# Performance work log

Measured on AMD Instinct MI355X. Metric: run time of the kernel, lower is better.

## Reference

```python
import jax, jax.numpy as jnp
import numpy as np

IN_C, OUT_C, MX, MY = 64, 64, 32, 32
B, H, W = 16, 256, 256


def setup_inputs() -> dict:
    key = jax.random.key(0)
    k1, k2, k3 = jax.random.split(key, 3)
    scale = 1.0 / (IN_C * OUT_C)
    x = jax.random.normal(k1, (B, IN_C, H, W), dtype=jnp.float32)
    weight_real = scale * jax.random.normal(k2, (IN_C, OUT_C, MX, MY), dtype=jnp.float32)
    weight_imag = scale * jax.random.normal(k3, (IN_C, OUT_C, MX, MY), dtype=jnp.float32)
    return {"x": x, "weight_real": weight_real, "weight_imag": weight_imag}


def reference(x, weight_real, weight_imag):
    Bv, C, Hv, Wv = x.shape
    x_ft = jnp.fft.rfft2(x, norm="ortho")  # [B, C_in, H, W//2+1] complex64
    mx = min(MX, Hv)
    my = min(MY, Wv // 2 + 1)
    x_crop = x_ft[:, :, :mx, :my]
    w = (weight_real[:, :, :mx, :my] + 1j * weight_imag[:, :, :mx, :my]).astype(jnp.complex64)
    # complex contraction over in_channels: [B,i,x,y] x [i,o,x,y] -> [B,o,x,y]
    out_modes = jnp.einsum("bixy,ioxy->boxy", x_crop, w)
    out_ft = jnp.zeros((Bv, OUT_C, Hv, Wv // 2 + 1), dtype=jnp.complex64)
    out_ft = out_ft.at[:, :, :mx, :my].set(out_modes)
    return jnp.fft.irfft2(out_ft, s=(Hv, Wv), norm="ortho")
```

## Files before the change

### kernel.cpp

```cpp
#include <hip/hip_runtime.h>
#include <math.h>


typedef _Float16 f16x4 __attribute__((ext_vector_type(4)));
typedef _Float16 f16x8 __attribute__((ext_vector_type(8)));
typedef float f32x4 __attribute__((ext_vector_type(4)));

__global__ __launch_bounds__(256) void k_tables(float* __restrict__ ws) {
    int idx = blockIdx.x * 256 + threadIdx.x;
    const float STEP = 6.283185307179586f / 256.f;
    float s, c;
    {
        int kx = idx >> 8, h = idx & 255;
        int t = (kx * h) & 255;
        sincosf((float)t * STEP, &s, &c);
        ((float2*)(ws + 16384))[kx * 256 + h] = make_float2(c, s);
    }
    _Float16* e1h = (_Float16*)ws;
    _Float16* e1l = (_Float16*)(ws + 8192);
    _Float16* e2h = (_Float16*)(ws + 32768);
    _Float16* e2l = (_Float16*)(ws + 40960);
    if (idx < 2048) {
        int l = idx & 63, nt = (idx >> 6) & 3, kt = idx >> 8;
        int col = nt * 16 + (l & 15);
        int ky = col >> 1;
        int kb = kt * 32 + (l >> 4) * 8;
#pragma unroll
        for (int j = 0; j < 8; ++j) {
            int k = kb + j;
            int tt_ = (k * ky) & 255;
            sincosf((float)tt_ * STEP, &s, &c);
            float val = ((col & 1) ? -s : c) * 256.f;
            _Float16 h = (_Float16)val;
            e1h[idx * 8 + j] = h;
            e1l[idx * 8 + j] = (_Float16)(val - (float)h);
        }
    } else if (idx < 4096) {
        int i2 = idx - 2048;
        int l = i2 & 63, nt = (i2 >> 6) & 15, kt = i2 >> 10;
        int w = nt * 16 + (l & 15);
        int kb = kt * 32 + (l >> 4) * 8;
#pragma unroll
        for (int j = 0; j < 8; ++j) {
            int k = kb + j;
            int ky = k >> 1;
            int tt_ = (ky * w) & 255;
            sincosf((float)tt_ * STEP, &s, &c);
            float val = ((k & 1) ? -s : c) * 256.f;
            _Float16 h = (_Float16)val;
            e2h[i2 * 8 + j] = h;
            e2l[i2 * 8 + j] = (_Float16)(val - (float)h);
        }
    }
}

__global__ __launch_bounds__(256) void k_f1(const float* __restrict__ x,
                                            const _Float16* __restrict__ e1h,
                                            const _Float16* __restrict__ e1l,
                                            float* __restrict__ y) {
    __shared__ _Float16 Ah[128 * 40];
    __shared__ _Float16 Al[128 * 40];
    int t = threadIdx.x, lane = t & 63, wv = t >> 6;
    long row0 = (long)blockIdx.x * 128;
    f32x4 acc[2][4];
#pragma unroll
    for (int m = 0; m < 2; ++m)
#pragma unroll
        for (int n = 0; n < 4; ++n) acc[m][n] = (f32x4){0.f, 0.f, 0.f, 0.f};
    int abase = (wv * 32 + (lane & 15)) * 40 + (lane >> 4) * 8;

    for (int kt = 0; kt < 8; ++kt) {
#pragma unroll
        for (int n = 0; n < 4; ++n) {
            int f4 = t + n * 256;
            int r = f4 >> 3, c4 = f4 & 7;
            float4 v = *(const float4*)&x[(row0 + r) * 256 + kt * 32 + c4 * 4];
            float s0 = v.x * 256.f, s1 = v.y * 256.f, s2 = v.z * 256.f, s3 = v.w * 256.f;
            _Float16 h0 = (_Float16)s0, h1 = (_Float16)s1;
            _Float16 h2 = (_Float16)s2, h3 = (_Float16)s3;
            *(f16x4*)&Ah[r * 40 + c4 * 4] = (f16x4){h0, h1, h2, h3};
            *(f16x4*)&Al[r * 40 + c4 * 4] =
                (f16x4){(_Float16)(s0 - (float)h0), (_Float16)(s1 - (float)h1),
                        (_Float16)(s2 - (float)h2), (_Float16)(s3 - (float)h3)};
        }
        __syncthreads();
        f16x8 ah0 = *(const f16x8*)&Ah[abase];
        f16x8 ah1 = *(const f16x8*)&Ah[abase + 16 * 40];
        f16x8 al0 = *(const f16x8*)&Al[abase];
        f16x8 al1 = *(const f16x8*)&Al[abase + 16 * 40];
#pragma unroll
        for (int n = 0; n < 4; ++n) {
            f16x8 bh = *(const f16x8*)(e1h + ((kt * 4 + n) * 64 + lane) * 8);
            f16x8 bl = *(const f16x8*)(e1l + ((kt * 4 + n) * 64 + lane) * 8);
            acc[0][n] = __builtin_amdgcn_mfma_f32_16x16x32_f16(ah0, bh, acc[0][n], 0, 0, 0);
            acc[0][n] = __builtin_amdgcn_mfma_f32_16x16x32_f16(al0, bh, acc[0][n], 0, 0, 0);
            acc[0][n] = __builtin_amdgcn_mfma_f32_16x16x32_f16(ah0, bl, acc[0][n], 0, 0, 0);
            acc[1][n] = __builtin_amdgcn_mfma_f32_16x16x32_f16(ah1, bh, acc[1][n], 0, 0, 0);
            acc[1][n] = __builtin_amdgcn_mfma_f32_16x16x32_f16(al1, bh, acc[1][n], 0, 0, 0);
            acc[1][n] = __builtin_amdgcn_mfma_f32_16x16x32_f16(ah1, bl, acc[1][n], 0, 0, 0);
        }
        __syncthreads();
    }
    const float SC = 1.f / 16777216.f;
#pragma unroll
    for (int m = 0; m < 2; ++m)
#pragma unroll
        for (int n = 0; n < 4; ++n)
#pragma unroll
            for (int r = 0; r < 4; ++r) {
                long row = row0 + wv * 32 + m * 16 + (lane >> 4) * 4 + r;
                y[row * 64 + n * 16 + (lane & 15)] = acc[m][n][r] * SC;
            }
}

__global__ __launch_bounds__(256) void k_f2(const float2* __restrict__ tt,
                                            const float2* __restrict__ y,
                                            float2* __restrict__ xf) {
    __shared__ float smem[2176 + 2048];
    float* As = smem;
    float* Bs = smem + 2176;
    int t = threadIdx.x, tx = t & 15, ty = t >> 4;
    int batch = blockIdx.x;
    const float2* ybase = y + (long)batch * 256 * 32;
    float acc[4][4];
#pragma unroll
    for (int i = 0; i < 4; ++i)
#pragma unroll
        for (int j = 0; j < 4; ++j) acc[i][j] = 0.f;

    for (int ht = 0; ht < 8; ++ht) {
        int h0 = ht * 32;
#pragma unroll
        for (int n = 0; n < 4; ++n) {
            int i2 = t + n * 256;
            int kx = i2 >> 5, hh = i2 & 31;
            float2 cs = tt[kx * 256 + h0 + hh];
            As[hh * 68 + kx] = cs.x;
            As[hh * 68 + 32 + kx] = cs.y;
        }
#pragma unroll
        for (int n = 0; n < 4; ++n) {
            int i2 = t + n * 256;
            int hh = i2 >> 5, ky = i2 & 31;
            float2 v = ybase[(h0 + hh) * 32 + ky];
            *(float2*)&Bs[hh * 64 + 2 * ky] = v;
        }
        __syncthreads();
#pragma unroll
        for (int kk = 0; kk < 32; ++kk) {
            float4 a0 = *(const float4*)&As[kk * 68 + ty * 4];
            float4 b0 = *(const float4*)&Bs[kk * 64 + tx * 4];
            float av[4] = {a0.x, a0.y, a0.z, a0.w};
            float bv[4] = {b0.x, b0.y, b0.z, b0.w};
#pragma unroll
            for (int i = 0; i < 4; ++i)
#pragma unroll
                for (int j = 0; j < 4; ++j)
                    acc[i][j] = fmaf(av[i], bv[j], acc[i][j]);
        }
        __syncthreads();
    }
    float* Cs = smem;
#pragma unroll
    for (int i = 0; i < 4; ++i)
#pragma unroll
        for (int j = 0; j < 4; ++j)
            Cs[(ty * 4 + i) * 65 + tx * 4 + j] = acc[i][j];
    __syncthreads();
#pragma unroll
    for (int n = 0; n < 4; ++n) {
        int idx = t + n * 256;
        int kx = idx >> 5, ky = idx & 31;
        float re = Cs[kx * 65 + 2 * ky]     + Cs[(kx + 32) * 65 + 2 * ky + 1];
        float im = Cs[kx * 65 + 2 * ky + 1] - Cs[(kx + 32) * 65 + 2 * ky];
        xf[(long)batch * 1024 + kx * 32 + ky] = make_float2(re, im);
    }
}

__global__ __launch_bounds__(256) void k_mix(const float* __restrict__ wr,
                                             const float* __restrict__ wi,
                                             const float2* __restrict__ xf,
                                             float2* __restrict__ om) {
    __shared__ float2 xs[64 * 32];
    int t = threadIdx.x;
    int b = blockIdx.x >> 5, kx = blockIdx.x & 31;
#pragma unroll
    for (int n = 0; n < 8; ++n) {
        int i2 = t + n * 256;
        int i = i2 >> 5, ky = i2 & 31;
        xs[i2] = xf[(long)(b * 64 + i) * 1024 + kx * 32 + ky];
    }
    __syncthreads();
    int ky = t & 31, og = t >> 5;
    float ar[8], ai[8];
#pragma unroll
    for (int j = 0; j < 8; ++j) { ar[j] = 0.f; ai[j] = 0.f; }
    const float* wrb = wr + kx * 32 + ky;
    const float* wib = wi + kx * 32 + ky;
    for (int i = 0; i < 64; ++i) {
        float2 xv = xs[i * 32 + ky];
#pragma unroll
        for (int j = 0; j < 8; ++j) {
            int o = og * 8 + j;
            long woff = (long)(i * 64 + o) * 1024;
            float wrv = wrb[woff], wiv = wib[woff];
            ar[j] = fmaf(xv.x, wrv, fmaf(-xv.y, wiv, ar[j]));
            ai[j] = fmaf(xv.x, wiv, fmaf(xv.y, wrv, ai[j]));
        }
    }
    float2* omb = om + (long)(b * 64) * 1024 + kx * 32 + ky;
#pragma unroll
    for (int j = 0; j < 8; ++j) {
        int o = og * 8 + j;
        omb[(long)o * 1024] = make_float2(ar[j], ai[j]);
    }
}

__global__ __launch_bounds__(256) void k_i1(const float2* __restrict__ tt,
                                            const float2* __restrict__ om,
                                            float2* __restrict__ g) {
    __shared__ float As[64 * 68];
    __shared__ float Bs[64 * 64];
    int t = threadIdx.x, tx = t & 15, ty = t >> 4;
    int bo = blockIdx.x >> 2, hb = blockIdx.x & 3;
    int h0 = hb * 64;
#pragma unroll
    for (int n = 0; n < 8; ++n) {
        int i2 = t + n * 256;
        int kx = i2 >> 6, hh = i2 & 63;
        float2 cs = tt[kx * 256 + h0 + hh];
        As[kx * 68 + hh] = cs.x;
        As[(kx + 32) * 68 + hh] = cs.y;
    }
    const float2* ombase = om + (long)bo * 1024;
#pragma unroll
    for (int n = 0; n < 4; ++n) {
        int i2 = t + n * 256;
        int kx = i2 >> 5, ky = i2 & 31;
        float2 v = ombase[kx * 32 + ky];
        Bs[kx * 64 + 2 * ky] = v.x;
        Bs[kx * 64 + 2 * ky + 1] = v.y;
        Bs[(kx + 32) * 64 + 2 * ky] = -v.y;
        Bs[(kx + 32) * 64 + 2 * ky + 1] = v.x;
    }
    __syncthreads();
    float acc[4][4];
#pragma unroll
    for (int i = 0; i < 4; ++i)
#pragma unroll
        for (int j = 0; j < 4; ++j) acc[i][j] = 0.f;
#pragma unroll 16
    for (int k = 0; k < 64; ++k) {
        float4 a0 = *(const float4*)&As[k * 68 + ty * 4];
        float4 b0 = *(const float4*)&Bs[k * 64 + tx * 4];
        float av[4] = {a0.x, a0.y, a0.z, a0.w};
        float bv[4] = {b0.x, b0.y, b0.z, b0.w};
#pragma unroll
        for (int i = 0; i < 4; ++i)
#pragma unroll
            for (int j = 0; j < 4; ++j)
                acc[i][j] = fmaf(av[i], bv[j], acc[i][j]);
    }
    float2* gbase = g + (long)bo * 256 * 32;
    float sa = (tx == 0) ? 1.f : 2.f;
#pragma unroll
    for (int i = 0; i < 4; ++i) {
        float4 v = make_float4(acc[i][0] * sa, acc[i][1] * sa, acc[i][2] * 2.f, acc[i][3] * 2.f);
        *(float4*)&gbase[(h0 + ty * 4 + i) * 32 + tx * 2] = v;
    }
}

__global__ __launch_bounds__(256) void k_i2(const float* __restrict__ g,
                                            const _Float16* __restrict__ e2h,
                                            const _Float16* __restrict__ e2l,
                                            float* __restrict__ out) {
    __shared__ _Float16 Ah[32 * 72];
    __shared__ _Float16 Al[32 * 72];
    int t = threadIdx.x, lane = t & 63, wv = t >> 6;
    long row0 = (long)blockIdx.x * 32;
#pragma unroll
    for (int n = 0; n < 2; ++n) {
        int f4 = t + n * 256;
        int r = f4 >> 4, c4 = f4 & 15;
        float4 v = *(const float4*)&g[(row0 + r) * 64 + c4 * 4];
        float s0 = v.x * 256.f, s1 = v.y * 256.f, s2 = v.z * 256.f, s3 = v.w * 256.f;
        _Float16 h0 = (_Float16)s0, h1 = (_Float16)s1;
        _Float16 h2 = (_Float16)s2, h3 = (_Float16)s3;
        *(f16x4*)&Ah[r * 72 + c4 * 4] = (f16x4){h0, h1, h2, h3};
        *(f16x4*)&Al[r * 72 + c4 * 4] =
            (f16x4){(_Float16)(s0 - (float)h0), (_Float16)(s1 - (float)h1),
                    (_Float16)(s2 - (float)h2), (_Float16)(s3 - (float)h3)};
    }
    __syncthreads();
    f32x4 acc[2][4];
#pragma unroll
    for (int m = 0; m < 2; ++m)
#pragma unroll
        for (int n = 0; n < 4; ++n) acc[m][n] = (f32x4){0.f, 0.f, 0.f, 0.f};
#pragma unroll
    for (int kt = 0; kt < 2; ++kt) {
        int abase = (lane & 15) * 72 + kt * 32 + (lane >> 4) * 8;
        f16x8 ah0 = *(const f16x8*)&Ah[abase];
        f16x8 ah1 = *(const f16x8*)&Ah[abase + 16 * 72];
        f16x8 al0 = *(const f16x8*)&Al[abase];
        f16x8 al1 = *(const f16x8*)&Al[abase + 16 * 72];
#pragma unroll
        for (int n = 0; n < 4; ++n) {
            int nb = ((kt * 16 + wv * 4 + n) * 64 + lane) * 8;
            f16x8 bh = *(const f16x8*)(e2h + nb);
            f16x8 bl = *(const f16x8*)(e2l + nb);
            acc[0][n] = __builtin_amdgcn_mfma_f32_16x16x32_f16(ah0, bh, acc[0][n], 0, 0, 0);
            acc[0][n] = __builtin_amdgcn_mfma_f32_16x16x32_f16(al0, bh, acc[0][n], 0, 0, 0);
            acc[0][n] = __builtin_amdgcn_mfma_f32_16x16x32_f16(ah0, bl, acc[0][n], 0, 0, 0);
            acc[1][n] = __builtin_amdgcn_mfma_f32_16x16x32_f16(ah1, bh, acc[1][n], 0, 0, 0);
            acc[1][n] = __builtin_amdgcn_mfma_f32_16x16x32_f16(al1, bh, acc[1][n], 0, 0, 0);
            acc[1][n] = __builtin_amdgcn_mfma_f32_16x16x32_f16(ah1, bl, acc[1][n], 0, 0, 0);
        }
    }
    const float SC = 1.f / 16777216.f;
#pragma unroll
    for (int m = 0; m < 2; ++m)
#pragma unroll
        for (int n = 0; n < 4; ++n)
#pragma unroll
            for (int r = 0; r < 4; ++r) {
                long row = row0 + m * 16 + (lane >> 4) * 4 + r;
                out[row * 256 + wv * 64 + n * 16 + (lane & 15)] = acc[m][n][r] * SC;
            }
}

extern "C" void kernel_launch(void* const* d_in, const int* in_sizes, int n_in,
                              void* d_out, int out_size, void* d_ws, size_t ws_size,
                              hipStream_t stream) {
    const float* x  = (const float*)d_in[0];
    const float* wr = (const float*)d_in[1];
    const float* wi = (const float*)d_in[2];
    float* out = (float*)d_out;
    float* ws = (float*)d_ws;

    const _Float16* e1h = (const _Float16*)ws;
    const _Float16* e1l = (const _Float16*)(ws + 8192);
    float2* tt = (float2*)(ws + 16384);
    const _Float16* e2h = (const _Float16*)(ws + 32768);
    const _Float16* e2l = (const _Float16*)(ws + 40960);
    float* y  = ws + 65536;
    float* xf = ws + 65536 + 16777216;
    float* om = ws + 65536 + 16777216 + 2097152;
    float* g  = y;

    hipLaunchKernelGGL(k_tables, dim3(32),   dim3(256), 0, stream, ws);
    hipLaunchKernelGGL(k_f1,     dim3(2048), dim3(256), 0, stream, x, e1h, e1l, y);
    hipLaunchKernelGGL(k_f2,     dim3(1024), dim3(256), 0, stream, tt, (const float2*)y, (float2*)xf);
    hipLaunchKernelGGL(k_mix,    dim3(512),  dim3(256), 0, stream, wr, wi, (const float2*)xf, (float2*)om);
    hipLaunchKernelGGL(k_i1,     dim3(4096), dim3(256), 0, stream, tt, (const float2*)om, (float2*)g);
    hipLaunchKernelGGL(k_i2,     dim3(8192), dim3(256), 0, stream, g, e2h, e2l, out);
}
```

Measured before the change: 613.0 us.

## Move H-axis DFT stages to split-fp16 MFMA and load A fragments directly

The second forward DFT stage and the first inverse stage move from scalar FP32 FMA GEMMs to fp16 hi/lo split MFMA GEMMs. k_tables now builds four precomputed twiddle tables in fragment layout. k_f1 writes its intermediate transposed (column-major over H) through shared memory so k_f2 can load contiguous K slices. k_f1 and k_i2 now load A fragments straight from global memory and split them in registers, which removes the shared-memory staging and barriers. The split-precision approach adds extra MFMA passes and carries some accuracy risk from fp16 rounding of the intermediates.

```diff
diff --git a/kernel.cpp b/kernel.cpp
--- a/kernel.cpp
+++ b/kernel.cpp
@@ -2,92 +2,105 @@
 #include <math.h>
 
 
-typedef _Float16 f16x4 __attribute__((ext_vector_type(4)));
 typedef _Float16 f16x8 __attribute__((ext_vector_type(8)));
 typedef float f32x4 __attribute__((ext_vector_type(4)));
 
+__device__ __forceinline__ void splitv(float s, _Float16& h, _Float16& l) {
+    h = (_Float16)s;
+    l = (_Float16)(s - (float)h);
+}
+
+__device__ __forceinline__ void split8(float4 a, float4 b, float sc, f16x8& hv, f16x8& lv) {
+    float v[8] = {a.x * sc, a.y * sc, a.z * sc, a.w * sc,
+                  b.x * sc, b.y * sc, b.z * sc, b.w * sc};
+#pragma unroll
+    for (int q = 0; q < 8; ++q) {
+        _Float16 h, l;
+        splitv(v[q], h, l);
+        hv[q] = h;
+        lv[q] = l;
+    }
+}
+
 __global__ __launch_bounds__(256) void k_tables(float* __restrict__ ws) {
     int idx = blockIdx.x * 256 + threadIdx.x;
+    int tab = idx >> 11, e = idx & 2047;
+    int l = e & 63;
     const float STEP = 6.283185307179586f / 256.f;
     float s, c;
-    {
-        int kx = idx >> 8, h = idx & 255;
-        int t = (kx * h) & 255;
-        sincosf((float)t * STEP, &s, &c);
-        ((float2*)(ws + 16384))[kx * 256 + h] = make_float2(c, s);
-    }
-    _Float16* e1h = (_Float16*)ws;
-    _Float16* e1l = (_Float16*)(ws + 8192);
-    _Float16* e2h = (_Float16*)(ws + 32768);
-    _Float16* e2l = (_Float16*)(ws + 40960);
-    if (idx < 2048) {
-        int l = idx & 63, nt = (idx >> 6) & 3, kt = idx >> 8;
-        int col = nt * 16 + (l & 15);
-        int ky = col >> 1;
-        int kb = kt * 32 + (l >> 4) * 8;
-#pragma unroll
-        for (int j = 0; j < 8; ++j) {
-            int k = kb + j;
-            int tt_ = (k * ky) & 255;
-            sincosf((float)tt_ * STEP, &s, &c);
-            float val = ((col & 1) ? -s : c) * 256.f;
-            _Float16 h = (_Float16)val;
-            e1h[idx * 8 + j] = h;
-            e1l[idx * 8 + j] = (_Float16)(val - (float)h);
-        }
-    } else if (idx < 4096) {
-        int i2 = idx - 2048;
-        int l = i2 & 63, nt = (i2 >> 6) & 15, kt = i2 >> 10;
-        int w = nt * 16 + (l & 15);
-        int kb = kt * 32 + (l >> 4) * 8;
-#pragma unroll
-        for (int j = 0; j < 8; ++j) {
-            int k = kb + j;
+    _Float16* hb;
+    _Float16* lb;
+    if (tab == 0) { hb = (_Float16*)ws;               lb = (_Float16*)(ws + 8192); }
+    else if (tab == 1) { hb = (_Float16*)(ws + 16384); lb = (_Float16*)(ws + 24576); }
+    else if (tab == 2) { hb = (_Float16*)(ws + 32768); lb = (_Float16*)(ws + 40960); }
+    else { hb = (_Float16*)(ws + 49152);               lb = (_Float16*)(ws + 57344); }
+#pragma unroll
+    for (int j = 0; j < 8; ++j) {
+        float val;
+        if (tab == 0) {
+            int nt = (e >> 6) & 3, kt = e >> 8;
+            int col = nt * 16 + (l & 15);
+            int ky = col >> 1;
+            int k = kt * 32 + (l >> 4) * 8 + j;
+            int t_ = (k * ky) & 255;
+            sincosf((float)t_ * STEP, &s, &c);
+            val = ((col & 1) ? -s : c) * 256.f;
+        } else if (tab == 1) {
+            int nt = (e >> 6) & 15, kt = e >> 10;
+            int w = nt * 16 + (l & 15);
+            int k = kt * 32 + (l >> 4) * 8 + j;
             int ky = k >> 1;
-            int tt_ = (ky * w) & 255;
-            sincosf((float)tt_ * STEP, &s, &c);
-            float val = ((k & 1) ? -s : c) * 256.f;
-            _Float16 h = (_Float16)val;
-            e2h[i2 * 8 + j] = h;
-            e2l[i2 * 8 + j] = (_Float16)(val - (float)h);
-        }
+            int t_ = (ky * w) & 255;
+            sincosf((float)t_ * STEP, &s, &c);
+            val = ((k & 1) ? -s : c) * 256.f;
+        } else if (tab == 2) {
+            int kt = (e >> 6) & 7, mt = e >> 9;
+            int m = mt * 16 + (l & 15);
+            int h = kt * 32 + (l >> 4) * 8 + j;
+            int mm = (m < 32) ? m : (m - 32);
+            int t_ = (mm * h) & 255;
+            sincosf((float)t_ * STEP, &s, &c);
+            val = ((m < 32) ? c : s) * 256.f;
+        } else {
+            int kt = (e >> 6) & 1, mt = e >> 7;
+            int h = mt * 16 + (l & 15);
+            int k = kt * 32 + (l >> 4) * 8 + j;
+            int kk = (k < 32) ? k : (k - 32);
+            int t_ = (kk * h) & 255;
+            sincosf((float)t_ * STEP, &s, &c);
+            val = ((k < 32) ? c : s) * 256.f;
+        }
+        _Float16 h16;
+        _Float16 l16;
+        splitv(val, h16, l16);
+        hb[e * 8 + j] = h16;
+        lb[e * 8 + j] = l16;
     }
 }
 
 __global__ __launch_bounds__(256) void k_f1(const float* __restrict__ x,
                                             const _Float16* __restrict__ e1h,
                                             const _Float16* __restrict__ e1l,
-                                            float* __restrict__ y) {
-    __shared__ _Float16 Ah[128 * 40];
-    __shared__ _Float16 Al[128 * 40];
+                                            float* __restrict__ yf) {
+    __shared__ float Ls[128 * 66];
     int t = threadIdx.x, lane = t & 63, wv = t >> 6;
     long row0 = (long)blockIdx.x * 128;
+    const float* xp0 = x + (row0 + wv * 32 + (lane & 15)) * 256 + (lane >> 4) * 8;
+    const float* xp1 = xp0 + 16 * 256;
     f32x4 acc[2][4];
 #pragma unroll
     for (int m = 0; m < 2; ++m)
 #pragma unroll
         for (int n = 0; n < 4; ++n) acc[m][n] = (f32x4){0.f, 0.f, 0.f, 0.f};
-    int abase = (wv * 32 + (lane & 15)) * 40 + (lane >> 4) * 8;
 
     for (int kt = 0; kt < 8; ++kt) {
-#pragma unroll
-        for (int n = 0; n < 4; ++n) {
-            int f4 = t + n * 256;
-            int r = f4 >> 3, c4 = f4 & 7;
-            float4 v = *(const float4*)&x[(row0 + r) * 256 + kt * 32 + c4 * 4];
-            float s0 = v.x * 256.f, s1 = v.y * 256.f, s2 = v.z * 256.f, s3 = v.w * 256.f;
-            _Float16 h0 = (_Float16)s0, h1 = (_Float16)s1;
-            _Float16 h2 = (_Float16)s2, h3 = (_Float16)s3;
-            *(f16x4*)&Ah[r * 40 + c4 * 4] = (f16x4){h0, h1, h2, h3};
-            *(f16x4*)&Al[r * 40 + c4 * 4] =
-                (f16x4){(_Float16)(s0 - (float)h0), (_Float16)(s1 - (float)h1),
-                        (_Float16)(s2 - (float)h2), (_Float16)(s3 - (float)h3)};
-        }
-        __syncthreads();
-        f16x8 ah0 = *(const f16x8*)&Ah[abase];
-        f16x8 ah1 = *(const f16x8*)&Ah[abase + 16 * 40];
-        f16x8 al0 = *(const f16x8*)&Al[abase];
-        f16x8 al1 = *(const f16x8*)&Al[abase + 16 * 40];
+        float4 a00 = *(const float4*)(xp0 + kt * 32);
+        float4 a01 = *(const float4*)(xp0 + kt * 32 + 4);
+        float4 a10 = *(const float4*)(xp1 + kt * 32);
+        float4 a11 = *(const float4*)(xp1 + kt * 32 + 4);
+        f16x8 ah0, al0, ah1, al1;
+        split8(a00, a01, 256.f, ah0, al0);
+        split8(a10, a11, 256.f, ah1, al1);
 #pragma unroll
         for (int n = 0; n < 4; ++n) {
             f16x8 bh = *(const f16x8*)(e1h + ((kt * 4 + n) * 64 + lane) * 8);
@@ -99,73 +112,73 @@
             acc[1][n] = __builtin_amdgcn_mfma_f32_16x16x32_f16(al1, bh, acc[1][n], 0, 0, 0);
             acc[1][n] = __builtin_amdgcn_mfma_f32_16x16x32_f16(ah1, bl, acc[1][n], 0, 0, 0);
         }
-        __syncthreads();
-    }
-    const float SC = 1.f / 16777216.f;
+    }
+    const float SCY = 1.f / 16777216.f;
 #pragma unroll
     for (int m = 0; m < 2; ++m)
 #pragma unroll
         for (int n = 0; n < 4; ++n)
 #pragma unroll
-            for (int r = 0; r < 4; ++r) {
-                long row = row0 + wv * 32 + m * 16 + (lane >> 4) * 4 + r;
-                y[row * 64 + n * 16 + (lane & 15)] = acc[m][n][r] * SC;
-            }
-}
-
-__global__ __launch_bounds__(256) void k_f2(const float2* __restrict__ tt,
-                                            const float2* __restrict__ y,
+            for (int r = 0; r < 4; ++r)
+                Ls[(wv * 32 + m * 16 + (lane >> 4) * 4 + r) * 66 + n * 16 + (lane & 15)] =
+                    acc[m][n][r] * SCY;
+    __syncthreads();
+    int col = t & 63, hg = t >> 6;
+    long bi = row0 >> 8;
+    int h0 = (int)(row0 & 255);
+    float* yp = yf + bi * 16384 + (long)col * 256 + h0 + hg * 32;
+#pragma unroll
+    for (int sseg = 0; sseg < 4; ++sseg) {
+        float4 v0, v1;
+        v0.x = Ls[(hg * 32 + sseg * 8 + 0) * 66 + col];
+        v0.y = Ls[(hg * 32 + sseg * 8 + 1) * 66 + col];
+        v0.z = Ls[(hg * 32 + sseg * 8 + 2) * 66 + col];
+        v0.w = Ls[(hg * 32 + sseg * 8 + 3) * 66 + col];
+        v1.x = Ls[(hg * 32 + sseg * 8 + 4) * 66 + col];
+        v1.y = Ls[(hg * 32 + sseg * 8 + 5) * 66 + col];
+        v1.z = Ls[(hg * 32 + sseg * 8 + 6) * 66 + col];
+        v1.w = Ls[(hg * 32 + sseg * 8 + 7) * 66 + col];
+        *(float4*)(yp + sseg * 8) = v0;
+        *(float4*)(yp + sseg * 8 + 4) = v1;
+    }
+}
+
+__global__ __launch_bounds__(256) void k_f2(const _Float16* __restrict__ t1h,
+                                            const _Float16* __restrict__ t1l,
+                                            const float* __restrict__ yf,
                                             float2* __restrict__ xf) {
-    __shared__ float smem[2176 + 2048];
-    float* As = smem;
-    float* Bs = smem + 2176;
-    int t = threadIdx.x, tx = t & 15, ty = t >> 4;
-    int batch = blockIdx.x;
-    const float2* ybase = y + (long)batch * 256 * 32;
-    float acc[4][4];
-#pragma unroll
-    for (int i = 0; i < 4; ++i)
-#pragma unroll
-        for (int j = 0; j < 4; ++j) acc[i][j] = 0.f;
-
-    for (int ht = 0; ht < 8; ++ht) {
-        int h0 = ht * 32;
+    __shared__ float Cs[64 * 65];
+    int t = threadIdx.x, lane = t & 63, wv = t >> 6;
+    long bi = blockIdx.x;
+    const float* yb = yf + bi * 16384;
+    f32x4 acc[4];
+#pragma unroll
+    for (int n = 0; n < 4; ++n) acc[n] = (f32x4){0.f, 0.f, 0.f, 0.f};
+
+    for (int kt = 0; kt < 8; ++kt) {
+        f16x8 ah = *(const f16x8*)(t1h + ((wv * 8 + kt) * 64 + lane) * 8);
+        f16x8 al = *(const f16x8*)(t1l + ((wv * 8 + kt) * 64 + lane) * 8);
+        int hoff = kt * 32 + (lane >> 4) * 8;
 #pragma unroll
         for (int n = 0; n < 4; ++n) {
-            int i2 = t + n * 256;
-            int kx = i2 >> 5, hh = i2 & 31;
-            float2 cs = tt[kx * 256 + h0 + hh];
-            As[hh * 68 + kx] = cs.x;
-            As[hh * 68 + 32 + kx] = cs.y;
-        }
-#pragma unroll
-        for (int n = 0; n < 4; ++n) {
-            int i2 = t + n * 256;
-            int hh = i2 >> 5, ky = i2 & 31;
-            float2 v = ybase[(h0 + hh) * 32 + ky];
-            *(float2*)&Bs[hh * 64 + 2 * ky] = v;
-        }
-        __syncthreads();
-#pragma unroll
-        for (int kk = 0; kk < 32; ++kk) {
-            float4 a0 = *(const float4*)&As[kk * 68 + ty * 4];
-            float4 b0 = *(const float4*)&Bs[kk * 64 + tx * 4];
-            float av[4] = {a0.x, a0.y, a0.z, a0.w};
-            float bv[4] = {b0.x, b0.y, b0.z, b0.w};
-#pragma unroll
-            for (int i = 0; i < 4; ++i)
-#pragma unroll
-                for (int j = 0; j < 4; ++j)
-                    acc[i][j] = fmaf(av[i], bv[j], acc[i][j]);
-        }
-        __syncthreads();
-    }
-    float* Cs = smem;
-#pragma unroll
-    for (int i = 0; i < 4; ++i)
-#pragma unroll
-        for (int j = 0; j < 4; ++j)
-            Cs[(ty * 4 + i) * 65 + tx * 4 + j] = acc[i][j];
+            int col = n * 16 + (lane & 15);
+            const float* p = yb + col * 256 + hoff;
+            float4 v0 = *(const float4*)p;
+            float4 v1 = *(const float4*)(p + 4);
+            f16x8 bh, bl;
+            split8(v0, v1, 1024.f, bh, bl);
+            acc[n] = __builtin_amdgcn_mfma_f32_16x16x32_f16(ah, bh, acc[n], 0, 0, 0);
+            acc[n] = __builtin_amdgcn_mfma_f32_16x16x32_f16(al, bh, acc[n], 0, 0, 0);
+            acc[n] = __builtin_amdgcn_mfma_f32_16x16x32_f16(ah, bl, acc[n], 0, 0, 0);
+            acc[n] = __builtin_amdgcn_mfma_f32_16x16x32_f16(al, bl, acc[n], 0, 0, 0);
+        }
+    }
+    const float SC = 1.f / 262144.f;
+#pragma unroll
+    for (int n = 0; n < 4; ++n)
+#pragma unroll
+        for (int r = 0; r < 4; ++r)
+            Cs[(wv * 16 + (lane >> 4) * 4 + r) * 65 + n * 16 + (lane & 15)] = acc[n][r] * SC;
     __syncthreads();
 #pragma unroll
     for (int n = 0; n < 4; ++n) {
@@ -173,7 +186,7 @@
         int kx = idx >> 5, ky = idx & 31;
         float re = Cs[kx * 65 + 2 * ky]     + Cs[(kx + 32) * 65 + 2 * ky + 1];
         float im = Cs[kx * 65 + 2 * ky + 1] - Cs[(kx + 32) * 65 + 2 * ky];
-        xf[(long)batch * 1024 + kx * 32 + ky] = make_float2(re, im);
+        xf[bi * 1024 + kx * 32 + ky] = make_float2(re, im);
     }
 }
 
@@ -216,82 +229,76 @@
     }
 }
 
-__global__ __launch_bounds__(256) void k_i1(const float2* __restrict__ tt,
+__global__ __launch_bounds__(256) void k_i1(const _Float16* __restrict__ t2h,
+                                            const _Float16* __restrict__ t2l,
                                             const float2* __restrict__ om,
-                                            float2* __restrict__ g) {
-    __shared__ float As[64 * 68];
-    __shared__ float Bs[64 * 64];
-    int t = threadIdx.x, tx = t & 15, ty = t >> 4;
-    int bo = blockIdx.x >> 2, hb = blockIdx.x & 3;
-    int h0 = hb * 64;
-#pragma unroll
-    for (int n = 0; n < 8; ++n) {
-        int i2 = t + n * 256;
-        int kx = i2 >> 6, hh = i2 & 63;
-        float2 cs = tt[kx * 256 + h0 + hh];
-        As[kx * 68 + hh] = cs.x;
-        As[(kx + 32) * 68 + hh] = cs.y;
-    }
-    const float2* ombase = om + (long)bo * 1024;
+                                            float* __restrict__ gf) {
+    __shared__ __align__(16) _Float16 Bsh[64 * 88];
+    __shared__ __align__(16) _Float16 Bsl[64 * 88];
+    int t = threadIdx.x, lane = t & 63, wv = t >> 6;
+    long bo = blockIdx.x;
+    const float2* omb = om + bo * 1024;
 #pragma unroll
     for (int n = 0; n < 4; ++n) {
-        int i2 = t + n * 256;
-        int kx = i2 >> 5, ky = i2 & 31;
-        float2 v = ombase[kx * 32 + ky];
-        Bs[kx * 64 + 2 * ky] = v.x;
-        Bs[kx * 64 + 2 * ky + 1] = v.y;
-        Bs[(kx + 32) * 64 + 2 * ky] = -v.y;
-        Bs[(kx + 32) * 64 + 2 * ky + 1] = v.x;
+        int e = t + n * 256;
+        int kx = e >> 5, ky = e & 31;
+        float2 v = omb[e];
+        float re = v.x * 4096.f, im = v.y * 4096.f;
+        _Float16 rh, rl, ih, il;
+        splitv(re, rh, rl);
+        splitv(im, ih, il);
+        Bsh[(2 * ky) * 88 + kx] = rh;          Bsl[(2 * ky) * 88 + kx] = rl;
+        Bsh[(2 * ky + 1) * 88 + kx] = ih;      Bsl[(2 * ky + 1) * 88 + kx] = il;
+        Bsh[(2 * ky) * 88 + kx + 32] = -ih;    Bsl[(2 * ky) * 88 + kx + 32] = -il;
+        Bsh[(2 * ky + 1) * 88 + kx + 32] = rh; Bsl[(2 * ky + 1) * 88 + kx + 32] = rl;
     }
     __syncthreads();
-    float acc[4][4];
-#pragma unroll
-    for (int i = 0; i < 4; ++i)
-#pragma unroll
-        for (int j = 0; j < 4; ++j) acc[i][j] = 0.f;
-#pragma unroll 16
-    for (int k = 0; k < 64; ++k) {
-        float4 a0 = *(const float4*)&As[k * 68 + ty * 4];
-        float4 b0 = *(const float4*)&Bs[k * 64 + tx * 4];
-        float av[4] = {a0.x, a0.y, a0.z, a0.w};
-        float bv[4] = {b0.x, b0.y, b0.z, b0.w};
-#pragma unroll
-        for (int i = 0; i < 4; ++i)
-#pragma unroll
-            for (int j = 0; j < 4; ++j)
-                acc[i][j] = fmaf(av[i], bv[j], acc[i][j]);
-    }
-    float2* gbase = g + (long)bo * 256 * 32;
-    float sa = (tx == 0) ? 1.f : 2.f;
-#pragma unroll
-    for (int i = 0; i < 4; ++i) {
-        float4 v = make_float4(acc[i][0] * sa, acc[i][1] * sa, acc[i][2] * 2.f, acc[i][3] * 2.f);
-        *(float4*)&gbase[(h0 + ty * 4 + i) * 32 + tx * 2] = v;
-    }
-}
-
-__global__ __launch_bounds__(256) void k_i2(const float* __restrict__ g,
+    f32x4 acc[4][4];
+#pragma unroll
+    for (int mi = 0; mi < 4; ++mi)
+#pragma unroll
+        for (int n = 0; n < 4; ++n) acc[mi][n] = (f32x4){0.f, 0.f, 0.f, 0.f};
+#pragma unroll
+    for (int mi = 0; mi < 4; ++mi) {
+        int mt = wv * 4 + mi;
+#pragma unroll
+        for (int kt = 0; kt < 2; ++kt) {
+            f16x8 ah = *(const f16x8*)(t2h + ((mt * 2 + kt) * 64 + lane) * 8);
+            f16x8 al = *(const f16x8*)(t2l + ((mt * 2 + kt) * 64 + lane) * 8);
+            int koff = kt * 32 + (lane >> 4) * 8;
+#pragma unroll
+            for (int n = 0; n < 4; ++n) {
+                int col = n * 16 + (lane & 15);
+                f16x8 bh = *(const f16x8*)&Bsh[col * 88 + koff];
+                f16x8 bl = *(const f16x8*)&Bsl[col * 88 + koff];
+                acc[mi][n] = __builtin_amdgcn_mfma_f32_16x16x32_f16(ah, bh, acc[mi][n], 0, 0, 0);
+                acc[mi][n] = __builtin_amdgcn_mfma_f32_16x16x32_f16(al, bh, acc[mi][n], 0, 0, 0);
+                acc[mi][n] = __builtin_amdgcn_mfma_f32_16x16x32_f16(ah, bl, acc[mi][n], 0, 0, 0);
+                acc[mi][n] = __builtin_amdgcn_mfma_f32_16x16x32_f16(al, bl, acc[mi][n], 0, 0, 0);
+            }
+        }
+    }
+#pragma unroll
+    for (int mi = 0; mi < 4; ++mi)
+#pragma unroll
+        for (int n = 0; n < 4; ++n) {
+            int col = n * 16 + (lane & 15);
+            float sa = ((col >> 1) == 0 ? 1.f : 2.f) * (1.f / 1048576.f);
+#pragma unroll
+            for (int r = 0; r < 4; ++r) {
+                int h = (wv * 4 + mi) * 16 + (lane >> 4) * 4 + r;
+                gf[bo * 16384 + h * 64 + col] = acc[mi][n][r] * sa;
+            }
+        }
+}
+
+__global__ __launch_bounds__(256) void k_i2(const float* __restrict__ gf,
                                             const _Float16* __restrict__ e2h,
                                             const _Float16* __restrict__ e2l,
                                             float* __restrict__ out) {
-    __shared__ _Float16 Ah[32 * 72];
-    __shared__ _Float16 Al[32 * 72];
     int t = threadIdx.x, lane = t & 63, wv = t >> 6;
     long row0 = (long)blockIdx.x * 32;
-#pragma unroll
-    for (int n = 0; n < 2; ++n) {
-        int f4 = t + n * 256;
-        int r = f4 >> 4, c4 = f4 & 15;
-        float4 v = *(const float4*)&g[(row0 + r) * 64 + c4 * 4];
-        float s0 = v.x * 256.f, s1 = v.y * 256.f, s2 = v.z * 256.f, s3 = v.w * 256.f;
-        _Float16 h0 = (_Float16)s0, h1 = (_Float16)s1;
-        _Float16 h2 = (_Float16)s2, h3 = (_Float16)s3;
-        *(f16x4*)&Ah[r * 72 + c4 * 4] = (f16x4){h0, h1, h2, h3};
-        *(f16x4*)&Al[r * 72 + c4 * 4] =
-            (f16x4){(_Float16)(s0 - (float)h0), (_Float16)(s1 - (float)h1),
-                    (_Float16)(s2 - (float)h2), (_Float16)(s3 - (float)h3)};
-    }
-    __syncthreads();
+    const float* gp0 = gf + (row0 + (lane & 15)) * 64 + (lane >> 4) * 8;
     f32x4 acc[2][4];
 #pragma unroll
     for (int m = 0; m < 2; ++m)
@@ -299,16 +306,17 @@
         for (int n = 0; n < 4; ++n) acc[m][n] = (f32x4){0.f, 0.f, 0.f, 0.f};
 #pragma unroll
     for (int kt = 0; kt < 2; ++kt) {
-        int abase = (lane & 15) * 72 + kt * 32 + (lane >> 4) * 8;
-        f16x8 ah0 = *(const f16x8*)&Ah[abase];
-        f16x8 ah1 = *(const f16x8*)&Ah[abase + 16 * 72];
-        f16x8 al0 = *(const f16x8*)&Al[abase];
-        f16x8 al1 = *(const f16x8*)&Al[abase + 16 * 72];
+        float4 v00 = *(const float4*)(gp0 + kt * 32);
+        float4 v01 = *(const float4*)(gp0 + kt * 32 + 4);
+        float4 v10 = *(const float4*)(gp0 + 16 * 64 + kt * 32);
+        float4 v11 = *(const float4*)(gp0 + 16 * 64 + kt * 32 + 4);
+        f16x8 ah0, al0, ah1, al1;
+        split8(v00, v01, 256.f, ah0, al0);
+        split8(v10, v11, 256.f, ah1, al1);
 #pragma unroll
         for (int n = 0; n < 4; ++n) {
-            int nb = ((kt * 16 + wv * 4 + n) * 64 + lane) * 8;
-            f16x8 bh = *(const f16x8*)(e2h + nb);
-            f16x8 bl = *(const f16x8*)(e2l + nb);
+            f16x8 bh = *(const f16x8*)(e2h + ((kt * 16 + wv * 4 + n) * 64 + lane) * 8);
+            f16x8 bl = *(const f16x8*)(e2l + ((kt * 16 + wv * 4 + n) * 64 + lane) * 8);
             acc[0][n] = __builtin_amdgcn_mfma_f32_16x16x32_f16(ah0, bh, acc[0][n], 0, 0, 0);
             acc[0][n] = __builtin_amdgcn_mfma_f32_16x16x32_f16(al0, bh, acc[0][n], 0, 0, 0);
             acc[0][n] = __builtin_amdgcn_mfma_f32_16x16x32_f16(ah0, bl, acc[0][n], 0, 0, 0);
@@ -340,18 +348,21 @@
 
     const _Float16* e1h = (const _Float16*)ws;
     const _Float16* e1l = (const _Float16*)(ws + 8192);
-    float2* tt = (float2*)(ws + 16384);
-    const _Float16* e2h = (const _Float16*)(ws + 32768);
-    const _Float16* e2l = (const _Float16*)(ws + 40960);
-    float* y  = ws + 65536;
-    float* xf = ws + 65536 + 16777216;
-    float* om = ws + 65536 + 16777216 + 2097152;
-    float* g  = y;
+    const _Float16* e2h = (const _Float16*)(ws + 16384);
+    const _Float16* e2l = (const _Float16*)(ws + 24576);
+    const _Float16* t1h = (const _Float16*)(ws + 32768);
+    const _Float16* t1l = (const _Float16*)(ws + 40960);
+    const _Float16* t2h = (const _Float16*)(ws + 49152);
+    const _Float16* t2l = (const _Float16*)(ws + 57344);
+    float* yf = ws + 65536;
+    float* xf = ws + 16842752;
+    float* om = ws + 18939904;
+    float* gf = yf;
 
     hipLaunchKernelGGL(k_tables, dim3(32),   dim3(256), 0, stream, ws);
-    hipLaunchKernelGGL(k_f1,     dim3(2048), dim3(256), 0, stream, x, e1h, e1l, y);
-    hipLaunchKernelGGL(k_f2,     dim3(1024), dim3(256), 0, stream, tt, (const float2*)y, (float2*)xf);
+    hipLaunchKernelGGL(k_f1,     dim3(2048), dim3(256), 0, stream, x, e1h, e1l, yf);
+    hipLaunchKernelGGL(k_f2,     dim3(1024), dim3(256), 0, stream, t1h, t1l, yf, (float2*)xf);
     hipLaunchKernelGGL(k_mix,    dim3(512),  dim3(256), 0, stream, wr, wi, (const float2*)xf, (float2*)om);
-    hipLaunchKernelGGL(k_i1,     dim3(4096), dim3(256), 0, stream, tt, (const float2*)om, (float2*)g);
-    hipLaunchKernelGGL(k_i2,     dim3(8192), dim3(256), 0, stream, g, e2h, e2l, out);
-}
+    hipLaunchKernelGGL(k_i1,     dim3(1024), dim3(256), 0, stream, t2h, t2l, (const float2*)om, gf);
+    hipLaunchKernelGGL(k_i2,     dim3(8192), dim3(256), 0, stream, gf, e2h, e2l, out);
+}
```

Measured after the change: 607.9 us. No clear change (-0.8%).
